# Performance work log

Measured on AMD Instinct MI355X. Metric: run time of the kernel, lower is better.

The kernel has to match this reference:

```python
import jax, jax.numpy as jnp
import numpy as np

H = 16  # heads
D = 1024  # hidden
HD = D // H
FF = 4096
EPS = 1e-12


def _linear_params(key, d_in, d_out):
    k1, k2 = jax.random.split(key)
    bound = 1.0 / np.sqrt(d_in)
    W = jax.random.uniform(k1, (d_in, d_out), minval=-bound, maxval=bound, dtype=jnp.float32)
    b = jax.random.uniform(k2, (d_out,), minval=-bound, maxval=bound, dtype=jnp.float32)
    return W, b


def setup_inputs() -> dict:
    key = jax.random.key(0)
    ks = jax.random.split(key, 8)
    x = jax.random.normal(ks[0], (4, 2048, D), dtype=jnp.float32)
    mask = jnp.ones((4, 1, 1, 2048), dtype=jnp.int32)
    Wq, bq = _linear_params(ks[1], D, D)
    Wk, bk = _linear_params(ks[2], D, D)
    Wv, bv = _linear_params(ks[3], D, D)
    Wo, bo = _linear_params(ks[4], D, D)
    W1, b1 = _linear_params(ks[5], D, FF)
    W2, b2 = _linear_params(ks[6], FF, D)
    g1 = jnp.ones((D,), jnp.float32); be1 = jnp.zeros((D,), jnp.float32)
    g2 = jnp.ones((D,), jnp.float32); be2 = jnp.zeros((D,), jnp.float32)
    return {"x": x, "mask": mask,
            "Wq": Wq, "bq": bq, "Wk": Wk, "bk": bk, "Wv": Wv, "bv": bv,
            "Wo": Wo, "bo": bo, "W1": W1, "b1": b1, "W2": W2, "b2": b2,
            "g1": g1, "be1": be1, "g2": g2, "be2": be2}


def _layernorm(x, g, b):
    mu = jnp.mean(x, axis=-1, keepdims=True)
    var = jnp.mean(jnp.square(x - mu), axis=-1, keepdims=True)
    return (x - mu) / jnp.sqrt(var + EPS) * g + b


def reference(x, mask, Wq, bq, Wk, bk, Wv, bv, Wo, bo, W1, b1, W2, b2, g1, be1, g2, be2):
    B, L, _ = x.shape
    h = _layernorm(x, g1, be1)
    # [B, H, L, HD]
    q = (h @ Wq + bq).reshape(B, L, H, HD).transpose(0, 2, 1, 3)
    k = (h @ Wk + bk).reshape(B, L, H, HD).transpose(0, 2, 1, 3)
    v = (h @ Wv + bv).reshape(B, L, H, HD).transpose(0, 2, 1, 3)
    scores = jnp.einsum('bhqd,bhkd->bhqk', q, k) / np.sqrt(HD).astype(np.float32)
    scores = jnp.where(mask == 0, jnp.float32(-1e9), scores)
    attn = jax.nn.softmax(scores, axis=-1)  # dropout = identity (eval mode)
    out = jnp.einsum('bhqk,bhkd->bhqd', attn, v)
    out = out.transpose(0, 2, 1, 3).reshape(B, L, D)
    x = x + (out @ Wo + bo)
    h = _layernorm(x, g2, be2)
    ff = jax.nn.gelu(h @ W1 + b1, approximate=False) @ W2 + b2
    return x + ff
```

## Files before the change

### kernel.cpp

```cpp
#include <hip/hip_runtime.h>
#include <stdint.h>

#define D_MODEL 1024
#define NHEAD   16
#define HDIM    64
#define FFDIM   4096
#define BATCH   4
#define SEQ     2048
#define ROWS    (BATCH*SEQ)

typedef unsigned short u16;
typedef __bf16 bf16_t;
typedef bf16_t bf16x8 __attribute__((ext_vector_type(8)));
typedef float  f32x4  __attribute__((ext_vector_type(4)));
typedef float  f32x16 __attribute__((ext_vector_type(16)));

#define SCQ 0.18033688011112042f

__device__ __forceinline__ u16 f2bf(float f) {
  union { float f; unsigned u; } v; v.f = f;
  unsigned r = v.u + 0x7fffu + ((v.u >> 16) & 1u);
  return (u16)(r >> 16);
}

__device__ __forceinline__ void gl2lds16(const void* g, void* l) {
  __builtin_amdgcn_global_load_lds((const __attribute__((address_space(1))) void*)g,
                                   (__attribute__((address_space(3))) void*)l, 16, 0, 0);
}

#define MFMA_BF16(a, b, c) __builtin_amdgcn_mfma_f32_16x16x32_bf16((a), (b), (c), 0, 0, 0)
#define MFMA32(a, b, c)    __builtin_amdgcn_mfma_f32_32x32x16_bf16((a), (b), (c), 0, 0, 0)
#define EXP2(x) __builtin_amdgcn_exp2f(x)

__device__ __forceinline__ bf16x8 mk8(unsigned a, unsigned b, unsigned c, unsigned d) {
  union { unsigned u[4]; bf16x8 v; } t;
  t.u[0] = a; t.u[1] = b; t.u[2] = c; t.u[3] = d;
  return t.v;
}

__global__ __launch_bounds__(256) void ln_kernel(const float* __restrict__ x,
                                                 const float* __restrict__ g,
                                                 const float* __restrict__ be,
                                                 u16* __restrict__ out) {
  __shared__ float red[10];
  int row = blockIdx.x;
  int t = threadIdx.x;
  const float* xr = x + (size_t)row * D_MODEL;
  float4 xv = ((const float4*)xr)[t];
  float s  = xv.x + xv.y + xv.z + xv.w;
  float s2 = xv.x*xv.x + xv.y*xv.y + xv.z*xv.z + xv.w*xv.w;
  for (int d = 32; d > 0; d >>= 1) { s += __shfl_down(s, d); s2 += __shfl_down(s2, d); }
  int wid = t >> 6;
  if ((t & 63) == 0) { red[wid*2] = s; red[wid*2+1] = s2; }
  __syncthreads();
  if (t == 0) {
    float a = 0.f, b2 = 0.f;
    for (int i = 0; i < 4; ++i) { a += red[i*2]; b2 += red[i*2+1]; }
    red[8] = a; red[9] = b2;
  }
  __syncthreads();
  float mu  = red[8] * (1.0f / D_MODEL);
  float var = red[9] * (1.0f / D_MODEL) - mu*mu;
  float rstd = rsqrtf(var + 1e-12f);
  float4 gv = ((const float4*)g)[t];
  float4 bv = ((const float4*)be)[t];
  unsigned long long o =
      (unsigned long long)f2bf((xv.x - mu) * rstd * gv.x + bv.x)
    | ((unsigned long long)f2bf((xv.y - mu) * rstd * gv.y + bv.y) << 16)
    | ((unsigned long long)f2bf((xv.z - mu) * rstd * gv.z + bv.z) << 32)
    | ((unsigned long long)f2bf((xv.w - mu) * rstd * gv.w + bv.w) << 48);
  ((unsigned long long*)out)[(size_t)row * (D_MODEL/4) + t] = o;
}

__global__ __launch_bounds__(256) void wt_kernel(const float* __restrict__ W,
                                                 u16* __restrict__ Wt, int K, int N) {
  __shared__ float tile[32][33];
  int n0 = blockIdx.x * 32, k0 = blockIdx.y * 32;
  int tx = threadIdx.x & 31, ty = threadIdx.x >> 5;
  #pragma unroll
  for (int i = 0; i < 4; ++i) {
    int k = ty + i*8;
    tile[k][tx] = W[(size_t)(k0 + k) * N + n0 + tx];
  }
  __syncthreads();
  #pragma unroll
  for (int i = 0; i < 4; ++i) {
    int n = ty + i*8;
    Wt[(size_t)(n0 + n) * K + k0 + tx] = f2bf(tile[tx][n]);
  }
}

__global__ __launch_bounds__(256) void vtrans_kernel(const u16* __restrict__ vb,
                                                     u16* __restrict__ vt) {
  __shared__ __align__(16) u16 tile[64][80];
  int kb = blockIdx.x * 64;
  int bh = blockIdx.y;
  int b = bh >> 4, h = bh & 15;
  int t = threadIdx.x;
  int key = t >> 2, dq = (t & 3) * 16;
  const u16* src = vb + (size_t)b*SEQ*D_MODEL + (size_t)(kb+key)*D_MODEL + h*HDIM + dq;
  *(bf16x8*)&tile[key][dq]     = *(const bf16x8*)(src);
  *(bf16x8*)&tile[key][dq + 8] = *(const bf16x8*)(src + 8);
  __syncthreads();
  int w = t >> 6, lane = t & 63;
  int kq = w * 16;
  u16 vals[16];
  #pragma unroll
  for (int e = 0; e < 16; ++e) vals[e] = tile[kq + e][lane];
  u16* dst = vt + (size_t)bh * HDIM * SEQ + (size_t)lane * SEQ + kb + kq;
  *(bf16x8*)dst       = *(const bf16x8*)&vals[0];
  *(bf16x8*)(dst + 8) = *(const bf16x8*)&vals[8];
}

__device__ __forceinline__ float gelu_f(float v) {
  return 0.5f * v * (1.0f + erff(v * 0.70710678118654752f));
}

template<int EPI>
__global__ __launch_bounds__(256) void gemm_bt(const u16* __restrict__ A,
                                               const u16* __restrict__ Bt,
                                               const float* __restrict__ bias,
                                               const float* __restrict__ resid,
                                               void* __restrict__ outp,
                                               int M, int N, int K,
                                               const float* __restrict__ bias2,
                                               const float* __restrict__ bias3,
                                               void* __restrict__ out2,
                                               void* __restrict__ out3) {
  __shared__ __align__(16) u16 sA[128*32];
  __shared__ __align__(16) u16 sB[128*32];
  const int tid = threadIdx.x;
  const int lane = tid & 63, w = tid >> 6;
  const int r = lane & 15, kg = lane >> 4;
  const int ks = kg ^ (r & 3);
  const int wr = w >> 1, wc = w & 1;

  const int gx = gridDim.x;
  const int nwg = gx * gridDim.y;
  const int orig = blockIdx.y * gx + blockIdx.x;
  const int lid = (orig & 7) * (nwg >> 3) + (orig >> 3);
  const int bm = lid / gx, bn = lid % gx;

  int row0 = tid >> 2, g0 = tid & 3;
  int row1 = 64 + row0;
  int c0 = (g0 ^ (row0 & 3)) * 8;
  int c1 = (g0 ^ (row1 & 3)) * 8;
  const u16* Ag0 = A  + (size_t)(bm*128 + row0) * K + c0;
  const u16* Ag1 = A  + (size_t)(bm*128 + row1) * K + c1;
  const u16* Bg0 = Bt + (size_t)(bn*128 + row0) * K + c0;
  const u16* Bg1 = Bt + (size_t)(bn*128 + row1) * K + c1;
  u16* lA0 = sA + tid*8;
  u16* lA1 = sA + (256 + tid)*8;
  u16* lB0 = sB + tid*8;
  u16* lB1 = sB + (256 + tid)*8;

  f32x4 acc[4][4];
  #pragma unroll
  for (int m = 0; m < 4; ++m)
    #pragma unroll
    for (int n = 0; n < 4; ++n) acc[m][n] = f32x4{0.f, 0.f, 0.f, 0.f};

  const float* bsel = bias;
  u16* osel = (u16*)outp;
  int bnl = bn;
  float qscale = 1.0f;
  if (EPI == 3) {
    int sec = bn >> 3;
    bsel = (sec == 0) ? bias : (sec == 1 ? bias2 : bias3);
    osel = (u16*)((sec == 0) ? outp : (sec == 1 ? out2 : out3));
    if (sec == 0) qscale = SCQ;
    bnl = bn & 7;
  }
  float bv4[4];
  #pragma unroll
  for (int n = 0; n < 4; ++n) bv4[n] = bsel[bnl*128 + wc*64 + n*16 + r];

  for (int k0 = 0; k0 < K; k0 += 32) {
    gl2lds16(Ag0 + k0, lA0);
    gl2lds16(Ag1 + k0, lA1);
    gl2lds16(Bg0 + k0, lB0);
    gl2lds16(Bg1 + k0, lB1);
    __syncthreads();
    bf16x8 af[4], bfr[4];
    #pragma unroll
    for (int m = 0; m < 4; ++m) af[m]  = *(const bf16x8*)&sA[(wr*64 + m*16 + r)*32 + ks*8];
    #pragma unroll
    for (int n = 0; n < 4; ++n) bfr[n] = *(const bf16x8*)&sB[(wc*64 + n*16 + r)*32 + ks*8];
    __builtin_amdgcn_s_setprio(1);
    #pragma unroll
    for (int m = 0; m < 4; ++m)
      #pragma unroll
      for (int n = 0; n < 4; ++n)
        acc[m][n] = MFMA_BF16(af[m], bfr[n], acc[m][n]);
    __builtin_amdgcn_s_setprio(0);
    __syncthreads();
  }

  const int orow = bm*128 + wr*64;
  const int ocol = (EPI == 3 ? bnl : bn)*128 + wc*64;
  const int ostride = (EPI == 3) ? 1024 : N;
  #pragma unroll
  for (int m = 0; m < 4; ++m) {
    #pragma unroll
    for (int n = 0; n < 4; ++n) {
      #pragma unroll
      for (int j = 0; j < 4; ++j) {
        int rr = orow + m*16 + kg*4 + j;
        int cc = ocol + n*16 + r;
        size_t idx = (size_t)rr * ostride + cc;
        float v = acc[m][n][j] + bv4[n];
        if (EPI == 0)       ((u16*)outp)[idx]   = f2bf(v);
        else if (EPI == 1)  ((float*)outp)[idx] = resid[idx] + v;
        else if (EPI == 2)  ((u16*)outp)[idx]   = f2bf(gelu_f(v));
        else                osel[idx]           = f2bf(v * qscale);
      }
    }
  }
}

__global__ __launch_bounds__(256, 4) void attn_kernel(const u16* __restrict__ qb,
                                                      const u16* __restrict__ kb,
                                                      const u16* __restrict__ vt,
                                                      const int* __restrict__ mask,
                                                      u16* __restrict__ ob) {
  __shared__ __align__(16) u16 sK[2][64*64];
  __shared__ __align__(16) u16 sV[2][64*64];
  __shared__ float sAl[4][32];
  __shared__ unsigned char sOkPart[256];
  __shared__ unsigned sTileOk;
  const float THR2 = 11.541560327111708f;
  int tid = threadIdx.x;
  int lane = tid & 63, w = tid >> 6;
  int l31 = lane & 31, hi = lane >> 5;
  int qt = blockIdx.x;
  int bh = blockIdx.y;
  int b = bh >> 4, h = bh & 15;
  size_t qkbase = (size_t)b * SEQ * D_MODEL + (size_t)h * HDIM;
  const u16* vtb = vt + (size_t)bh * HDIM * SEQ;
  const int* mrow = mask + b * SEQ;

  {
    int ok = 1;
    #pragma unroll
    for (int e = 0; e < 8; ++e) ok &= (mrow[tid*8 + e] != 0);
    sOkPart[tid] = (unsigned char)ok;
  }
  __syncthreads();
  if (w == 0) {
    int a = 0;
    if (lane < 32) {
      a = 1;
      #pragma unroll
      for (int e = 0; e < 8; ++e) a &= sOkPart[lane*8 + e];
    }
    unsigned long long bits = __ballot(a != 0);
    if (lane == 0) sTileOk = (unsigned)(bits & 0xffffffffu);
  }
  __syncthreads();
  const unsigned tileOkBits = sTileOk;

  const u16* qrow = qb + qkbase + (size_t)(qt*128 + w*32 + l31) * D_MODEL + hi*8;
  bf16x8 qf[4];
  #pragma unroll
  for (int dstep = 0; dstep < 4; ++dstep)
    qf[dstep] = *(const bf16x8*)(qrow + dstep*16);

  f32x16 oacc0, oacc1;
  #pragma unroll
  for (int e = 0; e < 16; ++e) { oacc0[e] = 0.f; oacc1[e] = 0.f; }
  float m_run = -1e30f;
  float lsum  = 0.f;

  int ch0 = w*64 + lane, ch1 = ch0 + 256;
  int row0 = ch0 >> 3, col0 = ((ch0 & 7) ^ (row0 & 7)) * 8;
  int row1 = ch1 >> 3, col1 = ((ch1 & 7) ^ (row1 & 7)) * 8;
  const u16* kp0 = kb + qkbase + (size_t)row0 * D_MODEL + col0;
  const u16* kp1 = kb + qkbase + (size_t)row1 * D_MODEL + col1;
  const u16* vp0 = vtb + (size_t)row0 * SEQ + col0;
  const u16* vp1 = vtb + (size_t)row1 * SEQ + col1;

  const int NT = SEQ / 64;

  gl2lds16(kp0, &sK[0][ch0*8]);
  gl2lds16(kp1, &sK[0][ch1*8]);
  gl2lds16(vp0, &sV[0][ch0*8]);
  gl2lds16(vp1, &sV[0][ch1*8]);
  kp0 += 64*D_MODEL; kp1 += 64*D_MODEL; vp0 += 64; vp1 += 64;

  for (int kt = 0; kt < NT; ++kt) {
    int cur = kt & 1;
    int key0 = kt * 64;
    if (kt + 1 < NT) {
      gl2lds16(kp0, &sK[cur^1][ch0*8]);
      gl2lds16(kp1, &sK[cur^1][ch1*8]);
      gl2lds16(vp0, &sV[cur^1][ch0*8]);
      gl2lds16(vp1, &sV[cur^1][ch1*8]);
      kp0 += 64*D_MODEL; kp1 += 64*D_MODEL; vp0 += 64; vp1 += 64;
      asm volatile("s_waitcnt vmcnt(4)" ::: "memory");
    } else {
      asm volatile("s_waitcnt vmcnt(0)" ::: "memory");
    }
    __builtin_amdgcn_s_barrier();

    const u16* Kt = sK[cur];
    const u16* Vt = sV[cur];

    f32x16 s0, s1;
    #pragma unroll
    for (int e = 0; e < 16; ++e) { s0[e] = 0.f; s1[e] = 0.f; }
    #pragma unroll
    for (int dstep = 0; dstep < 4; ++dstep) {
      int g = dstep*2 + hi;
      bf16x8 kf0 = *(const bf16x8*)&Kt[l31*64        + ((g ^ (l31 & 7)) * 8)];
      bf16x8 kf1 = *(const bf16x8*)&Kt[(32 + l31)*64 + ((g ^ ((32 + l31) & 7)) * 8)];
      s0 = MFMA32(kf0, qf[dstep], s0);
      s1 = MFMA32(kf1, qf[dstep], s1);
    }

    if (!((tileOkBits >> kt) & 1u)) {
      #pragma unroll
      for (int reg = 0; reg < 16; ++reg) {
        int kr = (reg & 3) + 8*(reg >> 2) + 4*hi;
        if (!mrow[key0 + kr])      s0[reg] = -1e9f;
        if (!mrow[key0 + 32 + kr]) s1[reg] = -1e9f;
      }
    }

    float tm = s0[0];
    #pragma unroll
    for (int e = 1; e < 16; ++e) tm = fmaxf(tm, s0[e]);
    #pragma unroll
    for (int e = 0; e < 16; ++e) tm = fmaxf(tm, s1[e]);
    tm = fmaxf(tm, __shfl_xor(tm, 32));

    if (__any(tm > m_run + THR2)) {
      float mn = fmaxf(m_run, tm);
      float al = EXP2(m_run - mn);
      m_run = mn;
      lsum *= al;
      if (lane < 32) sAl[w][lane] = al;
      asm volatile("s_waitcnt lgkmcnt(0)" ::: "memory");
      #pragma unroll
      for (int reg = 0; reg < 16; ++reg) {
        float a2 = sAl[w][(reg & 3) + 8*(reg >> 2) + 4*hi];
        oacc0[reg] *= a2; oacc1[reg] *= a2;
      }
    }

    #pragma unroll
    for (int e = 0; e < 16; ++e) {
      s0[e] = EXP2(s0[e] - m_run); lsum += s0[e];
      s1[e] = EXP2(s1[e] - m_run); lsum += s1[e];
    }

    unsigned wa, wb, wc, wd, we, wf, wg, wh;
#define CVTPK(dst, lo_, hi_) asm("v_cvt_pk_bf16_f32 %0, %1, %2" : "=v"(dst) : "v"(lo_), "v"(hi_))
    CVTPK(wa, s0[0],  s0[1]);  CVTPK(wb, s0[2],  s0[3]);
    CVTPK(wc, s0[4],  s0[5]);  CVTPK(wd, s0[6],  s0[7]);
    CVTPK(we, s0[8],  s0[9]);  CVTPK(wf, s0[10], s0[11]);
    CVTPK(wg, s0[12], s0[13]); CVTPK(wh, s0[14], s0[15]);
    asm volatile("v_permlane32_swap_b32 %0, %1" : "+v"(wc), "+v"(wa));
    asm volatile("v_permlane32_swap_b32 %0, %1" : "+v"(wd), "+v"(wb));
    asm volatile("v_permlane32_swap_b32 %0, %1" : "+v"(wg), "+v"(we));
    asm volatile("v_permlane32_swap_b32 %0, %1" : "+v"(wh), "+v"(wf));
    bf16x8 pa0 = mk8(wa, wb, wc, wd);
    bf16x8 pa1 = mk8(we, wf, wg, wh);
    CVTPK(wa, s1[0],  s1[1]);  CVTPK(wb, s1[2],  s1[3]);
    CVTPK(wc, s1[4],  s1[5]);  CVTPK(wd, s1[6],  s1[7]);
    CVTPK(we, s1[8],  s1[9]);  CVTPK(wf, s1[10], s1[11]);
    CVTPK(wg, s1[12], s1[13]); CVTPK(wh, s1[14], s1[15]);
    asm volatile("v_permlane32_swap_b32 %0, %1" : "+v"(wc), "+v"(wa));
    asm volatile("v_permlane32_swap_b32 %0, %1" : "+v"(wd), "+v"(wb));
    asm volatile("v_permlane32_swap_b32 %0, %1" : "+v"(wg), "+v"(we));
    asm volatile("v_permlane32_swap_b32 %0, %1" : "+v"(wh), "+v"(wf));
    bf16x8 pa2 = mk8(wa, wb, wc, wd);
    bf16x8 pa3 = mk8(we, wf, wg, wh);
#undef CVTPK

    int r0 = l31, r1 = 32 + l31;
    #pragma unroll
    for (int kstep = 0; kstep < 4; ++kstep) {
      int g = kstep*2 + hi;
      bf16x8 vf0 = *(const bf16x8*)&Vt[r0*64 + ((g ^ (r0 & 7)) * 8)];
      bf16x8 vf1 = *(const bf16x8*)&Vt[r1*64 + ((g ^ (r1 & 7)) * 8)];
      bf16x8 pk = (kstep == 0) ? pa0 : (kstep == 1) ? pa1 : (kstep == 2) ? pa2 : pa3;
      oacc0 = MFMA32(pk, vf0, oacc0);
      oacc1 = MFMA32(pk, vf1, oacc1);
    }
    __builtin_amdgcn_s_barrier();
  }

  float lsumT = lsum + __shfl_xor(lsum, 32);
  if (lane < 32) sAl[w][lane] = 1.0f / lsumT;
  asm volatile("s_waitcnt lgkmcnt(0)" ::: "memory");
  #pragma unroll
  for (int reg = 0; reg < 16; ++reg) {
    int qr = (reg & 3) + 8*(reg >> 2) + 4*hi;
    float rc = sAl[w][qr];
    int qg = qt*128 + w*32 + qr;
    size_t base2 = (size_t)(b*SEQ + qg) * D_MODEL + h*HDIM + l31;
    ob[base2]      = f2bf(oacc0[reg] * rc);
    ob[base2 + 32] = f2bf(oacc1[reg] * rc);
  }
}

extern "C" void kernel_launch(void* const* d_in, const int* in_sizes, int n_in,
                              void* d_out, int out_size, void* d_ws, size_t ws_size,
                              hipStream_t stream) {
  const float* x   = (const float*)d_in[0];
  const int*  mask = (const int*)d_in[1];
  const float* Wq = (const float*)d_in[2];  const float* bq = (const float*)d_in[3];
  const float* Wk = (const float*)d_in[4];  const float* bk = (const float*)d_in[5];
  const float* Wv = (const float*)d_in[6];  const float* bv = (const float*)d_in[7];
  const float* Wo = (const float*)d_in[8];  const float* bo = (const float*)d_in[9];
  const float* W1 = (const float*)d_in[10]; const float* b1 = (const float*)d_in[11];
  const float* W2 = (const float*)d_in[12]; const float* b2 = (const float*)d_in[13];
  const float* g1 = (const float*)d_in[14]; const float* be1 = (const float*)d_in[15];
  const float* g2 = (const float*)d_in[16]; const float* be2 = (const float*)d_in[17];

  const size_t MB = 1u << 20;
  char* ws = (char*)d_ws;
  u16*  hln  = (u16*)(ws);
  u16*  vt   = (u16*)(ws);
  u16*  qb   = (u16*)(ws + 16*MB);
  u16*  kb   = (u16*)(ws + 32*MB);
  u16*  vb   = (u16*)(ws + 48*MB);
  u16*  attn = (u16*)(ws + 64*MB);
  u16*  ff1  = (u16*)(ws + 16*MB);
  float* x2  = (float*)(ws + 80*MB);
  u16*  WqkvT= (u16*)(ws + 112*MB);
  u16*  WqT  = WqkvT;
  u16*  WkT  = (u16*)(ws + 114*MB);
  u16*  WvT  = (u16*)(ws + 116*MB);
  u16*  WoT  = (u16*)(ws + 118*MB);
  u16*  W1T  = (u16*)(ws + 120*MB);
  u16*  W2T  = (u16*)(ws + 128*MB);

  dim3 tb(256);
  wt_kernel<<<dim3(1024/32, 1024/32), tb, 0, stream>>>(Wq, WqT, 1024, 1024);
  wt_kernel<<<dim3(1024/32, 1024/32), tb, 0, stream>>>(Wk, WkT, 1024, 1024);
  wt_kernel<<<dim3(1024/32, 1024/32), tb, 0, stream>>>(Wv, WvT, 1024, 1024);
  wt_kernel<<<dim3(1024/32, 1024/32), tb, 0, stream>>>(Wo, WoT, 1024, 1024);
  wt_kernel<<<dim3(4096/32, 1024/32), tb, 0, stream>>>(W1, W1T, 1024, 4096);
  wt_kernel<<<dim3(1024/32, 4096/32), tb, 0, stream>>>(W2, W2T, 4096, 1024);

  ln_kernel<<<ROWS, tb, 0, stream>>>(x, g1, be1, hln);

  gemm_bt<3><<<dim3(3072/128, ROWS/128), tb, 0, stream>>>(hln, WqkvT, bq, nullptr, qb,
                                                          ROWS, 3072, 1024,
                                                          bk, bv, kb, vb);

  vtrans_kernel<<<dim3(SEQ/64, BATCH*NHEAD), tb, 0, stream>>>(vb, vt);

  attn_kernel<<<dim3(SEQ/128, BATCH*NHEAD), tb, 0, stream>>>(qb, kb, vt, mask, attn);

  gemm_bt<1><<<dim3(1024/128, ROWS/128), tb, 0, stream>>>(attn, WoT, bo, x, x2,
                                                          ROWS, 1024, 1024,
                                                          nullptr, nullptr, nullptr, nullptr);

  ln_kernel<<<ROWS, tb, 0, stream>>>(x2, g2, be2, hln);

  gemm_bt<2><<<dim3(4096/128, ROWS/128), tb, 0, stream>>>(hln, W1T, b1, nullptr, ff1,
                                                          ROWS, 4096, 1024,
                                                          nullptr, nullptr, nullptr, nullptr);

  gemm_bt<1><<<dim3(1024/128, ROWS/128), tb, 0, stream>>>(ff1, W2T, b2, x2, (float*)d_out,
                                                          ROWS, 1024, 4096,
                                                          nullptr, nullptr, nullptr, nullptr);
}
```

Measured before the change: 437.6 us.

## Replace GEMM with 256x256-tile, 8-wave, double-buffered ping-pong pipeline

Swaps the 128x128 single-buffered GEMM (4 waves, K-step 32) for a 256x256 tile kernel with 8 waves, K-step 64 and double-buffered LDS. Compute is split into eight phases per pair of K tiles, and each phase issues the global-to-LDS load for the next tile while running MFMAs on the current one. Raw s_barrier and explicit waitcnt calls sequence the two. The larger tile increases operand reuse and the overlap hides load latency. In exchange it uses about 128KB of LDS per block, grids become much smaller (e.g. 128 blocks for the N=1024 GEMMs on a 256-CU part), and workgroup mapping changes.

New measurement: 569.8 us. +30.2%, slower.

```diff
diff --git a/kernel.cpp b/kernel.cpp
--- a/kernel.cpp
+++ b/kernel.cpp
@@ -117,46 +117,52 @@
 }
 
 template<int EPI>
-__global__ __launch_bounds__(256) void gemm_bt(const u16* __restrict__ A,
-                                               const u16* __restrict__ Bt,
-                                               const float* __restrict__ bias,
-                                               const float* __restrict__ resid,
-                                               void* __restrict__ outp,
-                                               int M, int N, int K,
-                                               const float* __restrict__ bias2,
-                                               const float* __restrict__ bias3,
-                                               void* __restrict__ out2,
-                                               void* __restrict__ out3) {
-  __shared__ __align__(16) u16 sA[128*32];
-  __shared__ __align__(16) u16 sB[128*32];
+__global__ __launch_bounds__(512, 2) void gemm8p(const u16* __restrict__ A,
+                                                 const u16* __restrict__ Bt,
+                                                 const float* __restrict__ bias,
+                                                 const float* __restrict__ resid,
+                                                 void* __restrict__ outp,
+                                                 int M, int N, int K,
+                                                 const float* __restrict__ bias2,
+                                                 const float* __restrict__ bias3,
+                                                 void* __restrict__ out2,
+                                                 void* __restrict__ out3) {
+  __shared__ __align__(16) u16 sA[2][2][128*64];
+  __shared__ __align__(16) u16 sB[2][2][128*64];
   const int tid = threadIdx.x;
   const int lane = tid & 63, w = tid >> 6;
   const int r = lane & 15, kg = lane >> 4;
-  const int ks = kg ^ (r & 3);
-  const int wr = w >> 1, wc = w & 1;
-
-  const int gx = gridDim.x;
-  const int nwg = gx * gridDim.y;
+  const int wm = w >> 2, wn = w & 3;
+
+  const int gx = gridDim.x, gy = gridDim.y;
+  const int nwg = gx * gy;
   const int orig = blockIdx.y * gx + blockIdx.x;
   const int lid = (orig & 7) * (nwg >> 3) + (orig >> 3);
-  const int bm = lid / gx, bn = lid % gx;
-
-  int row0 = tid >> 2, g0 = tid & 3;
-  int row1 = 64 + row0;
-  int c0 = (g0 ^ (row0 & 3)) * 8;
-  int c1 = (g0 ^ (row1 & 3)) * 8;
-  const u16* Ag0 = A  + (size_t)(bm*128 + row0) * K + c0;
-  const u16* Ag1 = A  + (size_t)(bm*128 + row1) * K + c1;
-  const u16* Bg0 = Bt + (size_t)(bn*128 + row0) * K + c0;
-  const u16* Bg1 = Bt + (size_t)(bn*128 + row1) * K + c1;
-  u16* lA0 = sA + tid*8;
-  u16* lA1 = sA + (256 + tid)*8;
-  u16* lB0 = sB + tid*8;
-  u16* lB1 = sB + (256 + tid)*8;
-
-  f32x4 acc[4][4];
-  #pragma unroll
-  for (int m = 0; m < 4; ++m)
+  const int bm = lid % gy, bn = lid / gy;
+
+  size_t offA[2][2], offB[2][2];
+  #pragma unroll
+  for (int h = 0; h < 2; ++h) {
+    #pragma unroll
+    for (int u = 0; u < 2; ++u) {
+      int slot = u*512 + tid;
+      int lrow = slot >> 3, g = slot & 7;
+      int scol = (g ^ (lrow & 7)) * 8;
+      offA[h][u] = (size_t)(bm*256 + h*128 + lrow) * K + scol;
+      offB[h][u] = (size_t)(bn*256 + h*128 + lrow) * K + scol;
+    }
+  }
+
+#define STG_A(BUF, H, KT) { \
+    gl2lds16(A  + offA[H][0] + (size_t)(KT)*64, &sA[BUF][H][(0*512+tid)*8]); \
+    gl2lds16(A  + offA[H][1] + (size_t)(KT)*64, &sA[BUF][H][(1*512+tid)*8]); }
+#define STG_B(BUF, H, KT) { \
+    gl2lds16(Bt + offB[H][0] + (size_t)(KT)*64, &sB[BUF][H][(0*512+tid)*8]); \
+    gl2lds16(Bt + offB[H][1] + (size_t)(KT)*64, &sB[BUF][H][(1*512+tid)*8]); }
+
+  f32x4 acc[8][4];
+  #pragma unroll
+  for (int m = 0; m < 8; ++m)
     #pragma unroll
     for (int n = 0; n < 4; ++n) acc[m][n] = f32x4{0.f, 0.f, 0.f, 0.f};
 
@@ -165,48 +171,85 @@
   int bnl = bn;
   float qscale = 1.0f;
   if (EPI == 3) {
-    int sec = bn >> 3;
+    int sec = bn >> 2;
     bsel = (sec == 0) ? bias : (sec == 1 ? bias2 : bias3);
     osel = (u16*)((sec == 0) ? outp : (sec == 1 ? out2 : out3));
     if (sec == 0) qscale = SCQ;
-    bnl = bn & 7;
+    bnl = bn & 3;
   }
   float bv4[4];
   #pragma unroll
-  for (int n = 0; n < 4; ++n) bv4[n] = bsel[bnl*128 + wc*64 + n*16 + r];
-
-  for (int k0 = 0; k0 < K; k0 += 32) {
-    gl2lds16(Ag0 + k0, lA0);
-    gl2lds16(Ag1 + k0, lA1);
-    gl2lds16(Bg0 + k0, lB0);
-    gl2lds16(Bg1 + k0, lB1);
-    __syncthreads();
-    bf16x8 af[4], bfr[4];
-    #pragma unroll
-    for (int m = 0; m < 4; ++m) af[m]  = *(const bf16x8*)&sA[(wr*64 + m*16 + r)*32 + ks*8];
-    #pragma unroll
-    for (int n = 0; n < 4; ++n) bfr[n] = *(const bf16x8*)&sB[(wc*64 + n*16 + r)*32 + ks*8];
-    __builtin_amdgcn_s_setprio(1);
-    #pragma unroll
-    for (int m = 0; m < 4; ++m)
-      #pragma unroll
-      for (int n = 0; n < 4; ++n)
-        acc[m][n] = MFMA_BF16(af[m], bfr[n], acc[m][n]);
-    __builtin_amdgcn_s_setprio(0);
-    __syncthreads();
-  }
-
-  const int orow = bm*128 + wr*64;
-  const int ocol = (EPI == 3 ? bnl : bn)*128 + wc*64;
+  for (int n = 0; n < 4; ++n)
+    bv4[n] = bsel[bnl*256 + (n >> 1)*128 + wn*32 + (n & 1)*16 + r];
+
+#define PHASE(TB, MH, NH, STAGE_STMT, DO_VM0)                                  \
+  {                                                                            \
+    const u16* ha = sA[TB][MH];                                                \
+    const u16* hb = sB[TB][NH];                                                \
+    bf16x8 af[4][2], bfr[2][2];                                                \
+    _Pragma("unroll")                                                          \
+    for (int m2 = 0; m2 < 4; ++m2) {                                           \
+      int rowa = wm*64 + m2*16 + r;                                            \
+      af[m2][0] = *(const bf16x8*)&ha[rowa*64 + (((kg)     ^ (rowa & 7)) * 8)];\
+      af[m2][1] = *(const bf16x8*)&ha[rowa*64 + (((4 + kg) ^ (rowa & 7)) * 8)];\
+    }                                                                          \
+    _Pragma("unroll")                                                          \
+    for (int n2 = 0; n2 < 2; ++n2) {                                           \
+      int rowb = wn*32 + n2*16 + r;                                            \
+      bfr[n2][0] = *(const bf16x8*)&hb[rowb*64 + (((kg)     ^ (rowb & 7)) * 8)];\
+      bfr[n2][1] = *(const bf16x8*)&hb[rowb*64 + (((4 + kg) ^ (rowb & 7)) * 8)];\
+    }                                                                          \
+    STAGE_STMT;                                                                \
+    __builtin_amdgcn_s_barrier();                                              \
+    asm volatile("s_waitcnt lgkmcnt(0)" ::: "memory");                         \
+    __builtin_amdgcn_sched_barrier(0);                                         \
+    __builtin_amdgcn_s_setprio(1);                                             \
+    _Pragma("unroll")                                                          \
+    for (int m2 = 0; m2 < 4; ++m2) {                                           \
+      _Pragma("unroll")                                                        \
+      for (int n2 = 0; n2 < 2; ++n2) {                                         \
+        acc[(MH)*4+m2][(NH)*2+n2] =                                            \
+            MFMA_BF16(af[m2][0], bfr[n2][0], acc[(MH)*4+m2][(NH)*2+n2]);       \
+        acc[(MH)*4+m2][(NH)*2+n2] =                                            \
+            MFMA_BF16(af[m2][1], bfr[n2][1], acc[(MH)*4+m2][(NH)*2+n2]);       \
+      }                                                                        \
+    }                                                                          \
+    __builtin_amdgcn_s_setprio(0);                                             \
+    if (DO_VM0) asm volatile("s_waitcnt vmcnt(0)" ::: "memory");               \
+    __builtin_amdgcn_s_barrier();                                              \
+  }
+
+  STG_A(0, 0, 0); STG_B(0, 0, 0); STG_B(0, 1, 0); STG_A(0, 1, 0);
+  asm volatile("s_waitcnt vmcnt(0)" ::: "memory");
+  __builtin_amdgcn_s_barrier();
+
+  const int NT2 = K >> 7;
+  for (int i = 0; i < NT2; ++i) {
+    const int t1 = 2*i + 1, t2 = 2*i + 2;
+    const bool pre = (i + 1 < NT2);
+    PHASE(0, 0, 0, STG_A(1, 0, t1), false);
+    PHASE(0, 0, 1, STG_B(1, 0, t1), false);
+    PHASE(0, 1, 0, STG_B(1, 1, t1), false);
+    PHASE(0, 1, 1, STG_A(1, 1, t1), true);
+    PHASE(1, 0, 0, if (pre) STG_A(0, 0, t2), false);
+    PHASE(1, 0, 1, if (pre) STG_B(0, 0, t2), false);
+    PHASE(1, 1, 0, if (pre) STG_B(0, 1, t2), false);
+    PHASE(1, 1, 1, if (pre) STG_A(0, 1, t2), true);
+  }
+#undef PHASE
+#undef STG_A
+#undef STG_B
+
+  const int ocolb = (EPI == 3 ? bnl : bn) * 256;
   const int ostride = (EPI == 3) ? 1024 : N;
   #pragma unroll
-  for (int m = 0; m < 4; ++m) {
+  for (int m = 0; m < 8; ++m) {
     #pragma unroll
     for (int n = 0; n < 4; ++n) {
       #pragma unroll
       for (int j = 0; j < 4; ++j) {
-        int rr = orow + m*16 + kg*4 + j;
-        int cc = ocol + n*16 + r;
+        int rr = bm*256 + (m >> 2)*128 + wm*64 + (m & 3)*16 + kg*4 + j;
+        int cc = ocolb + (n >> 1)*128 + wn*32 + (n & 1)*16 + r;
         size_t idx = (size_t)rr * ostride + cc;
         float v = acc[m][n][j] + bv4[n];
         if (EPI == 0)       ((u16*)outp)[idx]   = f2bf(v);
@@ -446,25 +489,26 @@
 
   ln_kernel<<<ROWS, tb, 0, stream>>>(x, g1, be1, hln);
 
-  gemm_bt<3><<<dim3(3072/128, ROWS/128), tb, 0, stream>>>(hln, WqkvT, bq, nullptr, qb,
-                                                          ROWS, 3072, 1024,
-                                                          bk, bv, kb, vb);
+  dim3 gb(512);
+  gemm8p<3><<<dim3(3072/256, ROWS/256), gb, 0, stream>>>(hln, WqkvT, bq, nullptr, qb,
+                                                         ROWS, 3072, 1024,
+                                                         bk, bv, kb, vb);
 
   vtrans_kernel<<<dim3(SEQ/64, BATCH*NHEAD), tb, 0, stream>>>(vb, vt);
 
   attn_kernel<<<dim3(SEQ/128, BATCH*NHEAD), tb, 0, stream>>>(qb, kb, vt, mask, attn);
 
-  gemm_bt<1><<<dim3(1024/128, ROWS/128), tb, 0, stream>>>(attn, WoT, bo, x, x2,
-                                                          ROWS, 1024, 1024,
-                                                          nullptr, nullptr, nullptr, nullptr);
+  gemm8p<1><<<dim3(1024/256, ROWS/256), gb, 0, stream>>>(attn, WoT, bo, x, x2,
+                                                         ROWS, 1024, 1024,
+                                                         nullptr, nullptr, nullptr, nullptr);
 
   ln_kernel<<<ROWS, tb, 0, stream>>>(x2, g2, be2, hln);
 
-  gemm_bt<2><<<dim3(4096/128, ROWS/128), tb, 0, stream>>>(hln, W1T, b1, nullptr, ff1,
-                                                          ROWS, 4096, 1024,
-                                                          nullptr, nullptr, nullptr, nullptr);
-
-  gemm_bt<1><<<dim3(1024/128, ROWS/128), tb, 0, stream>>>(ff1, W2T, b2, x2, (float*)d_out,
-                                                          ROWS, 1024, 4096,
-                                                          nullptr, nullptr, nullptr, nullptr);
-}
+  gemm8p<2><<<dim3(4096/256, ROWS/256), gb, 0, stream>>>(hln, W1T, b1, nullptr, ff1,
+                                                         ROWS, 4096, 1024,
+                                                         nullptr, nullptr, nullptr, nullptr);
+
+  gemm8p<1><<<dim3(1024/256, ROWS/256), gb, 0, stream>>>(ff1, W2T, b2, x2, (float*)d_out,
+                                                         ROWS, 1024, 4096,
+                                                         nullptr, nullptr, nullptr, nullptr);
+}
```
